# Optimization experiments

Hardware: AMD Instinct MI355X
Metric: run time of the kernel (lower is better)

## Reference

```python
import jax, jax.numpy as jnp
import numpy as np

N_PATHS, SEQ_LEN = 8192, 512
DATA_DIM, HIDDEN = 2, 128
MIN_VOL, MAX_VOL = 1e-4, 5.0


def setup_inputs() -> dict:
    key = jax.random.key(0)
    ks = jax.random.split(key, 10)
    def w(k, fin, fout, scale=1.0):
        return (jax.random.normal(k, (fin, fout), jnp.float32) * (scale / np.sqrt(fin))).astype(jnp.float32)
    # diffusion output bias init from the torch module: log(exp(target_vol) - 1 + 1e-8)
    gb3_init = float(np.log(np.exp(0.1) - 1.0 + 1e-8))
    return {
        "y0": jax.random.normal(ks[0], (N_PATHS, DATA_DIM), jnp.float32) * 0.1,
        "ts": jnp.arange(SEQ_LEN, dtype=jnp.float32),  # dt = 1.0 between outputs
        "dW": jax.random.normal(ks[1], (SEQ_LEN - 1, N_PATHS, DATA_DIM), jnp.float32),
        "fw1": w(ks[2], DATA_DIM + 1, HIDDEN), "fb1": jnp.zeros((HIDDEN,), jnp.float32),
        "fw2": w(ks[3], HIDDEN, HIDDEN),       "fb2": jnp.zeros((HIDDEN,), jnp.float32),
        "fw3": w(ks[4], HIDDEN, DATA_DIM, 0.02), "fb3": jnp.zeros((DATA_DIM,), jnp.float32),
        "gw1": w(ks[5], DATA_DIM, HIDDEN),     "gb1": jnp.zeros((HIDDEN,), jnp.float32),
        "gw2": w(ks[6], HIDDEN, HIDDEN),       "gb2": jnp.zeros((HIDDEN,), jnp.float32),
        "gw3": w(ks[7], HIDDEN, DATA_DIM, 0.02),
        "gb3": jnp.full((DATA_DIM,), gb3_init, jnp.float32),
    }


def _sde_paths(y0, ts, dW, fw1, fb1, fw2, fb2, fw3, fb3, gw1, gb1, gw2, gb2, gw3, gb3):
    def drift(y):  # f(t, y): MLP on [y, spread]
        spread = y[:, 0:1] - y[:, 1:2]
        h = jnp.concatenate([y, spread], axis=-1)            # [N, D+1]
        h = jax.nn.silu(h @ fw1 + fb1)
        h = jax.nn.silu(h @ fw2 + fb2)
        return h @ fw3 + fb3                                  # [N, D]

    def diffusion(y):  # g(t, y): softplus + clamp
        h = jax.nn.silu(y @ gw1 + gb1)
        h = jax.nn.silu(h @ gw2 + gb2)
        raw = h @ gw3 + gb3
        return jnp.clip(jax.nn.softplus(raw), MIN_VOL, MAX_VOL)  # [N, D]

    dts = ts[1:] - ts[:-1]  # [T-1]

    def step(y, inp):
        dw_std, dt = inp
        dw = dw_std * jnp.sqrt(dt)                 # Brownian increment ~ N(0, dt)
        f = drift(y)
        g, vjp_g = jax.vjp(diffusion, y)
        v = 0.5 * (dw * dw - dt)                   # Milstein weight (Ito)
        corr = vjp_g(v * g)[0]                     # torchsde autograd gdg_prod
        y1 = y + f * dt + g * dw + corr
        return y1, y1

    _, ys = jax.lax.scan(step, y0, (dW, dts))      # ys: [T-1, N, D]
    paths = jnp.concatenate([y0[None], ys], axis=0)  # [T, N, D]
    return jnp.transpose(paths, (1, 0, 2))           # [N, T, D]


def reference(y0, ts, dW, fw1, fb1, fw2, fb2, fw3, fb3, gw1, gb1, gw2, gb2, gw3, gb3):
    return _sde_paths(y0, ts, dW, fw1, fb1, fw2, fb2, fw3, fb3,
                      gw1, gb1, gw2, gb2, gw3, gb3)
```

## Files before the change

### kernel.cpp

```cpp
#include <hip/hip_runtime.h>
#include <math.h>

#define H      128
#define NPATH  8192
#define TLEN   512
#define BP     32
#define NTHR   512

typedef short bf16x8 __attribute__((ext_vector_type(8)));
typedef float f32x4  __attribute__((ext_vector_type(4)));

#define MFMA(a,b,c) __builtin_amdgcn_mfma_f32_16x16x32_bf16((a),(b),(c),0,0,0)

#define BAR() asm volatile("s_waitcnt lgkmcnt(0)\n\ts_barrier" ::: "memory")

#define O_WF2T  0
#define O_WG2T  32768
#define O_WG2R  65536
#define O_BFH   98304
#define O_BFL   106496
#define O_BGH   114688
#define O_BGL   122880
#define O_PF    131072
#define O_PRAW  132096
#define O_PCORR 133120
#define O_EP    134144
#define EP_FB2   0
#define EP_GB2   512
#define EP_W3F0  1024
#define EP_W3F1  1536
#define EP_W3G0  2048
#define EP_W3G1  2560
#define EP_GW1B0 3072
#define EP_GW1B1 3584
#define EP_GB1B  4096
#define O_TS    138752
#define SMEM_BYTES (O_TS + TLEN*4)

__device__ __forceinline__ float bf2f(unsigned v){ return __uint_as_float(v << 16); }
__device__ __forceinline__ unsigned short f2bf(float f){
  unsigned u = __float_as_uint(f);
  return (unsigned short)((u + 0x7fffu + ((u >> 16) & 1u)) >> 16);
}
__device__ __forceinline__ float ldany(const void* p, long long i, bool isbf){
  return isbf ? bf2f(((const unsigned short*)p)[i]) : ((const float*)p)[i];
}
__device__ __forceinline__ unsigned short ldbf(const void* p, long long i, bool isbf){
  return isbf ? ((const unsigned short*)p)[i] : f2bf(((const float*)p)[i]);
}
__device__ __forceinline__ float fsig(float x){
  return __builtin_amdgcn_rcpf(1.0f + __expf(-x));
}
__device__ __forceinline__ float fsilu(float x){ return x * fsig(x); }
__device__ __forceinline__ float fsilud(float x){
  float s = fsig(x); return s * (1.0f + x * (1.0f - s));
}
__device__ __forceinline__ float fsoftplus(float x){
  if (x > 15.0f) return x;
  return __logf(1.0f + __expf(x));
}
__device__ __forceinline__ unsigned cvtpk(float a, float b){
  unsigned r; asm("v_cvt_pk_bf16_f32 %0, %1, %2" : "=v"(r) : "v"(a), "v"(b)); return r;
}
__device__ __forceinline__ bf16x8 asfrag(uint4 u){
  union { uint4 u; bf16x8 b; } v; v.u = u; return v.b;
}

__global__ __launch_bounds__(NTHR, 2)
void GeneratorSDE_kernel(const void* __restrict__ y0, const void* __restrict__ ts,
                         const void* __restrict__ dW,
                         const void* __restrict__ fw1, const void* __restrict__ fb1,
                         const void* __restrict__ fw2, const void* __restrict__ fb2,
                         const void* __restrict__ fw3, const void* __restrict__ fb3,
                         const void* __restrict__ gw1, const void* __restrict__ gb1,
                         const void* __restrict__ gw2, const void* __restrict__ gb2,
                         const void* __restrict__ gw3, const void* __restrict__ gb3,
                         void* __restrict__ out)
{
  extern __shared__ char sm[];
  const int tid  = threadIdx.x;
  const int lane = tid & 63;
  const int w    = tid >> 6;
  const int wp   = w >> 1;
  const int nt   = w & 1;
  const int m16  = lane & 15;
  const int q    = lane >> 4;
  const int gpb  = blockIdx.x * BP;
  const int p1   = nt*16 + m16;
  const int gp   = gpb + p1;
  const int k8   = wp*32 + q*8;

  const bool isbf = (((const unsigned*)ts)[1] != 0x3f800000u);

  const int RACT  = O_BFH + ((q*32 + p1) << 4);
  const int WACT  = O_BFH + (((wp*4 + q)*32 + p1) << 4);
  const int WC2   = O_BFH + (((wp*4 + (q >> 1))*32 + p1) << 4) + ((q & 1) << 3);
  const int RAW   = O_WF2T + ((q*128 + wp*32 + m16) << 4);
  const int RAR   = O_WG2R + ((q*128 + wp*32 + m16) << 4);
  const int RPART = O_PF + (p1 << 3);
  const int WPART = O_PF + ((wp*32 + p1) << 3);
  const int REP   = O_EP + wp*128 + q*16;

  for (int e = tid; e < H * H; e += NTHR){
    int k = e >> 7, n = e & 127;
    unsigned short fv = ldbf(fw2, e, isbf);
    unsigned short gv = ldbf(gw2, e, isbf);
    *(unsigned short*)(sm + O_WF2T + (((k >> 3)*128 + n) << 4) + ((k & 7) << 1)) = fv;
    *(unsigned short*)(sm + O_WG2T + (((k >> 3)*128 + n) << 4) + ((k & 7) << 1)) = gv;
    *(unsigned short*)(sm + O_WG2R + (((n >> 3)*128 + k) << 4) + ((n & 7) << 1)) = gv;
  }
  if (tid < H){
    int e = tid;
    ((float*)(sm + O_EP + EP_FB2))[e]   = ldany(fb2, e, isbf);
    ((float*)(sm + O_EP + EP_GB2))[e]   = ldany(gb2, e, isbf);
    ((float*)(sm + O_EP + EP_W3F0))[e]  = ldany(fw3, 2*e + 0, isbf);
    ((float*)(sm + O_EP + EP_W3F1))[e]  = ldany(fw3, 2*e + 1, isbf);
    ((float*)(sm + O_EP + EP_W3G0))[e]  = ldany(gw3, 2*e + 0, isbf);
    ((float*)(sm + O_EP + EP_W3G1))[e]  = ldany(gw3, 2*e + 1, isbf);
    ((float*)(sm + O_EP + EP_GW1B0))[e] = ldany(gw1, e, isbf);
    ((float*)(sm + O_EP + EP_GW1B1))[e] = ldany(gw1, H + e, isbf);
    ((float*)(sm + O_EP + EP_GB1B))[e]  = ldany(gb1, e, isbf);
  }
  for (int e = tid; e < TLEN; e += NTHR)
    ((float*)(sm + O_TS))[e] = ldany(ts, e, isbf);

  float fw1a[8], fw1b[8], fb1r[8], gw1r0[8], gw1r1[8], gb1r[8];
  #pragma unroll
  for (int kk = 0; kk < 8; ++kk){
    int k = k8 + kk;
    float r0 = ldany(fw1, k, isbf), r1 = ldany(fw1, H + k, isbf), r2 = ldany(fw1, 2*H + k, isbf);
    fw1a[kk]  = r0 + r2;
    fw1b[kk]  = r1 - r2;
    fb1r[kk]  = ldany(fb1, k,     isbf);
    gw1r0[kk] = ldany(gw1, k,     isbf);
    gw1r1[kk] = ldany(gw1, H + k, isbf);
    gb1r[kk]  = ldany(gb1, k,     isbf);
  }
  const float fb3r0 = ldany(fb3, 0, isbf), fb3r1 = ldany(fb3, 1, isbf);
  const float gb3r0 = ldany(gb3, 0, isbf), gb3r1 = ldany(gb3, 1, isbf);

  float ycur0 = ldany(y0, (long long)gp*2 + 0, isbf);
  float ycur1 = ldany(y0, (long long)gp*2 + 1, isbf);
  if (w < 2 && lane < 16){
    size_t r = (size_t)gp * TLEN;
    if (isbf) ((unsigned*)out)[r] = (unsigned)f2bf(ycur0) | ((unsigned)f2bf(ycur1) << 16);
    else      ((float2*)out)[r]   = make_float2(ycur0, ycur1);
  }
  float2 dwcur;
  {
    long long e = (long long)gp * 2;
    if (isbf){ unsigned u = *(const unsigned*)((const unsigned short*)dW + e);
               dwcur = make_float2(bf2f(u & 0xffffu), bf2f(u >> 16)); }
    else       dwcur = *(const float2*)((const float*)dW + e);
  }
  __syncthreads();

  const float* TSf = (const float*)(sm + O_TS);

  for (int t = 0; t < TLEN - 1; ++t){
    float dt = TSf[t+1] - TSf[t];
    float sqdt = sqrtf(dt);

    float2 dwnext;
    {
      int tn = (t + 1 <= TLEN - 2) ? t + 1 : TLEN - 2;
      long long e = ((long long)tn * NPATH + gp) * 2;
      if (isbf){ unsigned u = *(const unsigned*)((const unsigned short*)dW + e);
                 dwnext = make_float2(bf2f(u & 0xffffu), bf2f(u >> 16)); }
      else       dwnext = *(const float2*)((const float*)dW + e);
    }

    {
      float hf[8], hg[8];
      #pragma unroll
      for (int kk = 0; kk < 8; ++kk){
        hf[kk] = fsilu(fb1r[kk] + ycur0*fw1a[kk]  + ycur1*fw1b[kk]);
        hg[kk] = fsilu(gb1r[kk] + ycur0*gw1r0[kk] + ycur1*gw1r1[kk]);
      }
      unsigned fh[4], fl[4], gh[4], gl[4];
      #pragma unroll
      for (int i = 0; i < 4; ++i){
        fh[i] = cvtpk(hf[2*i], hf[2*i+1]);
        gh[i] = cvtpk(hg[2*i], hg[2*i+1]);
        float f0 = __uint_as_float(fh[i] << 16), f1 = __uint_as_float(fh[i] & 0xffff0000u);
        float g0 = __uint_as_float(gh[i] << 16), g1 = __uint_as_float(gh[i] & 0xffff0000u);
        fl[i] = cvtpk(hf[2*i] - f0, hf[2*i+1] - f1);
        gl[i] = cvtpk(hg[2*i] - g0, hg[2*i+1] - g1);
      }
      *(uint4*)(sm + WACT        ) = make_uint4(fh[0], fh[1], fh[2], fh[3]);
      *(uint4*)(sm + WACT +  8192) = make_uint4(fl[0], fl[1], fl[2], fl[3]);
      *(uint4*)(sm + WACT + 16384) = make_uint4(gh[0], gh[1], gh[2], gh[3]);
      *(uint4*)(sm + WACT + 24576) = make_uint4(gl[0], gl[1], gl[2], gl[3]);
    }
    BAR();

    f32x4 accg[2];
    float sgr[8];
    f32x4 w3g0v[2], w3g1v[2];
    {
      f32x4 accf[2];
      accf[0] = (f32x4)0.f; accf[1] = (f32x4)0.f;
      accg[0] = (f32x4)0.f; accg[1] = (f32x4)0.f;
      #pragma unroll
      for (int kt = 0; kt < 4; ++kt){
        bf16x8 bfh = asfrag(*(const uint4*)(sm + RACT + kt*2048        ));
        bf16x8 bfl = asfrag(*(const uint4*)(sm + RACT + kt*2048 +  8192));
        bf16x8 bgh = asfrag(*(const uint4*)(sm + RACT + kt*2048 + 16384));
        bf16x8 bgl = asfrag(*(const uint4*)(sm + RACT + kt*2048 + 24576));
        bf16x8 af0 = asfrag(*(const uint4*)(sm + RAW + kt*8192        ));
        bf16x8 af1 = asfrag(*(const uint4*)(sm + RAW + kt*8192 +   256));
        bf16x8 ag0 = asfrag(*(const uint4*)(sm + RAW + kt*8192 + 32768));
        bf16x8 ag1 = asfrag(*(const uint4*)(sm + RAW + kt*8192 + 33024));
        accf[0] = MFMA(af0, bfl, accf[0]); accf[0] = MFMA(af0, bfh, accf[0]);
        accf[1] = MFMA(af1, bfl, accf[1]); accf[1] = MFMA(af1, bfh, accf[1]);
        accg[0] = MFMA(ag0, bgl, accg[0]); accg[0] = MFMA(ag0, bgh, accg[0]);
        accg[1] = MFMA(ag1, bgl, accg[1]); accg[1] = MFMA(ag1, bgh, accg[1]);
      }
      float pf0 = 0, pf1 = 0, pr0 = 0, pr1 = 0;
      #pragma unroll
      for (int mi = 0; mi < 2; ++mi){
        f32x4 fb2v  = *(const f32x4*)(sm + REP + mi*64 + EP_FB2);
        f32x4 gb2v  = *(const f32x4*)(sm + REP + mi*64 + EP_GB2);
        f32x4 w3f0v = *(const f32x4*)(sm + REP + mi*64 + EP_W3F0);
        f32x4 w3f1v = *(const f32x4*)(sm + REP + mi*64 + EP_W3F1);
        w3g0v[mi] = *(const f32x4*)(sm + REP + mi*64 + EP_W3G0);
        w3g1v[mi] = *(const f32x4*)(sm + REP + mi*64 + EP_W3G1);
        #pragma unroll
        for (int r = 0; r < 4; ++r){
          float vf = fsilu(accf[mi][r] + fb2v[r]);
          pf0 += vf * w3f0v[r];
          pf1 += vf * w3f1v[r];
          float zg = accg[mi][r] + gb2v[r];
          float s  = fsig(zg);
          accg[mi][r] = zg;
          sgr[mi*4+r] = s;
          float vg = zg * s;
          pr0 += vg * w3g0v[mi][r];
          pr1 += vg * w3g1v[mi][r];
        }
      }
      pf0 += __shfl_xor(pf0, 16, 64); pf0 += __shfl_xor(pf0, 32, 64);
      pf1 += __shfl_xor(pf1, 16, 64); pf1 += __shfl_xor(pf1, 32, 64);
      pr0 += __shfl_xor(pr0, 16, 64); pr0 += __shfl_xor(pr0, 32, 64);
      pr1 += __shfl_xor(pr1, 16, 64); pr1 += __shfl_xor(pr1, 32, 64);
      if (lane < 16){
        *(float2*)(sm + WPART       ) = make_float2(pf0, pf1);
        *(float2*)(sm + WPART + 1024) = make_float2(pr0, pr1);
      }
    }
    BAR();

    float g0, g1, dw0, dw1, cr0, cr1;
    {
      float raw0 = gb3r0, raw1 = gb3r1;
      #pragma unroll
      for (int w2 = 0; w2 < 4; ++w2){
        float2 v = *(const float2*)(sm + RPART + w2*256 + 1024);
        raw0 += v.x; raw1 += v.y;
      }
      dw0 = dwcur.x * sqdt; dw1 = dwcur.y * sqdt;
      float vv0 = 0.5f*(dw0*dw0 - dt), vv1 = 0.5f*(dw1*dw1 - dt);
      float sp0 = fsoftplus(raw0), sp1 = fsoftplus(raw1);
      g0 = fminf(fmaxf(sp0, 1e-4f), 5.0f);
      g1 = fminf(fmaxf(sp1, 1e-4f), 5.0f);
      float m0 = (sp0 > 1e-4f && sp0 < 5.0f) ? 1.0f : 0.0f;
      float m1 = (sp1 > 1e-4f && sp1 < 5.0f) ? 1.0f : 0.0f;
      cr0 = vv0 * (g0 * fsig(raw0) * m0);
      cr1 = vv1 * (g1 * fsig(raw1) * m1);
    }

    #pragma unroll
    for (int mi = 0; mi < 2; ++mi){
      float c2[4];
      #pragma unroll
      for (int r = 0; r < 4; ++r){
        float s = sgr[mi*4+r], z = accg[mi][r];
        float sd = s * (1.0f + z * (1.0f - s));
        c2[r] = (cr0 * w3g0v[mi][r] + cr1 * w3g1v[mi][r]) * sd;
      }
      unsigned h0 = cvtpk(c2[0], c2[1]), h1 = cvtpk(c2[2], c2[3]);
      float a0 = __uint_as_float(h0 << 16), a1 = __uint_as_float(h0 & 0xffff0000u);
      float a2 = __uint_as_float(h1 << 16), a3 = __uint_as_float(h1 & 0xffff0000u);
      unsigned l0 = cvtpk(c2[0] - a0, c2[1] - a1), l1 = cvtpk(c2[2] - a2, c2[3] - a3);
      *(uint2*)(sm + WC2 + mi*1024       ) = make_uint2(h0, h1);
      *(uint2*)(sm + WC2 + mi*1024 + 8192) = make_uint2(l0, l1);
    }
    BAR();

    {
      f32x4 accc[2];
      accc[0] = (f32x4)0.f; accc[1] = (f32x4)0.f;
      #pragma unroll
      for (int kt = 0; kt < 4; ++kt){
        bf16x8 bh = asfrag(*(const uint4*)(sm + RACT + kt*2048       ));
        bf16x8 bl = asfrag(*(const uint4*)(sm + RACT + kt*2048 + 8192));
        bf16x8 a0 = asfrag(*(const uint4*)(sm + RAR + kt*8192      ));
        bf16x8 a1 = asfrag(*(const uint4*)(sm + RAR + kt*8192 + 256));
        accc[0] = MFMA(a0, bl, accc[0]); accc[0] = MFMA(a0, bh, accc[0]);
        accc[1] = MFMA(a1, bl, accc[1]); accc[1] = MFMA(a1, bh, accc[1]);
      }
      float pc0 = 0, pc1 = 0;
      #pragma unroll
      for (int mi = 0; mi < 2; ++mi){
        f32x4 gb1v = *(const f32x4*)(sm + REP + mi*64 + EP_GB1B );
        f32x4 b0v  = *(const f32x4*)(sm + REP + mi*64 + EP_GW1B0);
        f32x4 b1v  = *(const f32x4*)(sm + REP + mi*64 + EP_GW1B1);
        #pragma unroll
        for (int r = 0; r < 4; ++r){
          float z1 = gb1v[r] + ycur0*b0v[r] + ycur1*b1v[r];
          float u  = accc[mi][r] * fsilud(z1);
          pc0 += u * b0v[r];
          pc1 += u * b1v[r];
        }
      }
      pc0 += __shfl_xor(pc0, 16, 64); pc0 += __shfl_xor(pc0, 32, 64);
      pc1 += __shfl_xor(pc1, 16, 64); pc1 += __shfl_xor(pc1, 32, 64);
      if (lane < 16)
        *(float2*)(sm + WPART + 2048) = make_float2(pc0, pc1);
    }
    BAR();

    {
      float f0 = fb3r0, f1 = fb3r1, c0 = 0.f, c1 = 0.f;
      #pragma unroll
      for (int w2 = 0; w2 < 4; ++w2){
        float2 a = *(const float2*)(sm + RPART + w2*256       );
        float2 b = *(const float2*)(sm + RPART + w2*256 + 2048);
        f0 += a.x; f1 += a.y; c0 += b.x; c1 += b.y;
      }
      ycur0 += f0*dt + g0*dw0 + c0;
      ycur1 += f1*dt + g1*dw1 + c1;
      if (w < 2 && lane < 16){
        size_t r = (size_t)gp * TLEN + (t + 1);
        if (isbf) ((unsigned*)out)[r] = (unsigned)f2bf(ycur0) | ((unsigned)f2bf(ycur1) << 16);
        else      ((float2*)out)[r]   = make_float2(ycur0, ycur1);
      }
      dwcur = dwnext;
    }
  }
}

extern "C" void kernel_launch(void* const* d_in, const int* in_sizes, int n_in,
                              void* d_out, int out_size, void* d_ws, size_t ws_size,
                              hipStream_t stream)
{
  (void)in_sizes; (void)n_in; (void)out_size; (void)d_ws; (void)ws_size;
  hipFuncSetAttribute((const void*)GeneratorSDE_kernel,
                      hipFuncAttributeMaxDynamicSharedMemorySize, SMEM_BYTES);
  GeneratorSDE_kernel<<<dim3(NPATH / BP), dim3(NTHR), SMEM_BYTES, stream>>>(
      d_in[0], d_in[1], d_in[2],
      d_in[3], d_in[4], d_in[5], d_in[6], d_in[7], d_in[8],
      d_in[9], d_in[10], d_in[11], d_in[12], d_in[13], d_in[14],
      d_out);
}
```

Baseline: 2.146 ms.

## Keep MLP weight fragments in registers instead of shared memory

Loads the fw2, gw2 and transposed gw2 MFMA A-fragments once into per-thread registers (96 VGPRs) instead of staging them in LDS and re-reading them every timestep. LDS use drops by about 96KB and launch bounds go from two blocks per CU to one, so more registers are available. The aim is to remove per-step LDS weight traffic from the serial scan. The cost is lower occupancy and possible register spills. Initial weight loads become strided global reads.

```diff
diff --git a/kernel.cpp b/kernel.cpp
--- a/kernel.cpp
+++ b/kernel.cpp
@@ -14,17 +14,14 @@
 
 #define BAR() asm volatile("s_waitcnt lgkmcnt(0)\n\ts_barrier" ::: "memory")
 
-#define O_WF2T  0
-#define O_WG2T  32768
-#define O_WG2R  65536
-#define O_BFH   98304
-#define O_BFL   106496
-#define O_BGH   114688
-#define O_BGL   122880
-#define O_PF    131072
-#define O_PRAW  132096
-#define O_PCORR 133120
-#define O_EP    134144
+#define O_BFH   0
+#define O_BFL   8192
+#define O_BGH   16384
+#define O_BGL   24576
+#define O_PF    32768
+#define O_PRAW  33792
+#define O_PCORR 34816
+#define O_EP    35840
 #define EP_FB2   0
 #define EP_GB2   512
 #define EP_W3F0  1024
@@ -34,7 +31,7 @@
 #define EP_GW1B0 3072
 #define EP_GW1B1 3584
 #define EP_GB1B  4096
-#define O_TS    138752
+#define O_TS    40448
 #define SMEM_BYTES (O_TS + TLEN*4)
 
 __device__ __forceinline__ float bf2f(unsigned v){ return __uint_as_float(v << 16); }
@@ -66,7 +63,7 @@
   union { uint4 u; bf16x8 b; } v; v.u = u; return v.b;
 }
 
-__global__ __launch_bounds__(NTHR, 2)
+__global__ __launch_bounds__(NTHR, 1)
 void GeneratorSDE_kernel(const void* __restrict__ y0, const void* __restrict__ ts,
                          const void* __restrict__ dW,
                          const void* __restrict__ fw1, const void* __restrict__ fb1,
@@ -95,20 +92,25 @@
   const int RACT  = O_BFH + ((q*32 + p1) << 4);
   const int WACT  = O_BFH + (((wp*4 + q)*32 + p1) << 4);
   const int WC2   = O_BFH + (((wp*4 + (q >> 1))*32 + p1) << 4) + ((q & 1) << 3);
-  const int RAW   = O_WF2T + ((q*128 + wp*32 + m16) << 4);
-  const int RAR   = O_WG2R + ((q*128 + wp*32 + m16) << 4);
   const int RPART = O_PF + (p1 << 3);
   const int WPART = O_PF + ((wp*32 + p1) << 3);
   const int REP   = O_EP + wp*128 + q*16;
 
-  for (int e = tid; e < H * H; e += NTHR){
-    int k = e >> 7, n = e & 127;
-    unsigned short fv = ldbf(fw2, e, isbf);
-    unsigned short gv = ldbf(gw2, e, isbf);
-    *(unsigned short*)(sm + O_WF2T + (((k >> 3)*128 + n) << 4) + ((k & 7) << 1)) = fv;
-    *(unsigned short*)(sm + O_WG2T + (((k >> 3)*128 + n) << 4) + ((k & 7) << 1)) = gv;
-    *(unsigned short*)(sm + O_WG2R + (((n >> 3)*128 + k) << 4) + ((n & 7) << 1)) = gv;
-  }
+  bf16x8 aF[2][4], aG[2][4], aR[2][4];
+  #pragma unroll
+  for (int mi = 0; mi < 2; ++mi)
+    #pragma unroll
+    for (int kt = 0; kt < 4; ++kt){
+      int row = 32*wp + 16*mi + m16;
+      #pragma unroll
+      for (int j = 0; j < 8; ++j){
+        int col = kt*32 + q*8 + j;
+        aF[mi][kt][j] = (short)ldbf(fw2, (long long)col*H + row, isbf);
+        aG[mi][kt][j] = (short)ldbf(gw2, (long long)col*H + row, isbf);
+        aR[mi][kt][j] = (short)ldbf(gw2, (long long)row*H + col, isbf);
+      }
+    }
+
   if (tid < H){
     int e = tid;
     ((float*)(sm + O_EP + EP_FB2))[e]   = ldany(fb2, e, isbf);
@@ -207,14 +209,10 @@
         bf16x8 bfl = asfrag(*(const uint4*)(sm + RACT + kt*2048 +  8192));
         bf16x8 bgh = asfrag(*(const uint4*)(sm + RACT + kt*2048 + 16384));
         bf16x8 bgl = asfrag(*(const uint4*)(sm + RACT + kt*2048 + 24576));
-        bf16x8 af0 = asfrag(*(const uint4*)(sm + RAW + kt*8192        ));
-        bf16x8 af1 = asfrag(*(const uint4*)(sm + RAW + kt*8192 +   256));
-        bf16x8 ag0 = asfrag(*(const uint4*)(sm + RAW + kt*8192 + 32768));
-        bf16x8 ag1 = asfrag(*(const uint4*)(sm + RAW + kt*8192 + 33024));
-        accf[0] = MFMA(af0, bfl, accf[0]); accf[0] = MFMA(af0, bfh, accf[0]);
-        accf[1] = MFMA(af1, bfl, accf[1]); accf[1] = MFMA(af1, bfh, accf[1]);
-        accg[0] = MFMA(ag0, bgl, accg[0]); accg[0] = MFMA(ag0, bgh, accg[0]);
-        accg[1] = MFMA(ag1, bgl, accg[1]); accg[1] = MFMA(ag1, bgh, accg[1]);
+        accf[0] = MFMA(aF[0][kt], bfl, accf[0]); accf[0] = MFMA(aF[0][kt], bfh, accf[0]);
+        accf[1] = MFMA(aF[1][kt], bfl, accf[1]); accf[1] = MFMA(aF[1][kt], bfh, accf[1]);
+        accg[0] = MFMA(aG[0][kt], bgl, accg[0]); accg[0] = MFMA(aG[0][kt], bgh, accg[0]);
+        accg[1] = MFMA(aG[1][kt], bgl, accg[1]); accg[1] = MFMA(aG[1][kt], bgh, accg[1]);
       }
       float pf0 = 0, pf1 = 0, pr0 = 0, pr1 = 0;
       #pragma unroll
@@ -294,10 +292,8 @@
       for (int kt = 0; kt < 4; ++kt){
         bf16x8 bh = asfrag(*(const uint4*)(sm + RACT + kt*2048       ));
         bf16x8 bl = asfrag(*(const uint4*)(sm + RACT + kt*2048 + 8192));
-        bf16x8 a0 = asfrag(*(const uint4*)(sm + RAR + kt*8192      ));
-        bf16x8 a1 = asfrag(*(const uint4*)(sm + RAR + kt*8192 + 256));
-        accc[0] = MFMA(a0, bl, accc[0]); accc[0] = MFMA(a0, bh, accc[0]);
-        accc[1] = MFMA(a1, bl, accc[1]); accc[1] = MFMA(a1, bh, accc[1]);
+        accc[0] = MFMA(aR[0][kt], bl, accc[0]); accc[0] = MFMA(aR[0][kt], bh, accc[0]);
+        accc[1] = MFMA(aR[1][kt], bl, accc[1]); accc[1] = MFMA(aR[1][kt], bh, accc[1]);
       }
       float pc0 = 0, pc1 = 0;
       #pragma unroll
```

Result: faster. 2.021 ms (-5.8%).

## Reschedule per-step stages to drop a barrier and overlap drift MFMA

Applied to the files above, without the earlier changes.

The drift layer-2 MFMA moves after the diffusion head, so it runs in the barrier window alongside the softplus and correction work. The backward VJP matmul is reorganised so each wave reads only the correction vector it wrote itself. That removes one block barrier per time step, and silu-derivatives are precomputed in the first stage and staged in a new shared-memory region. Layer-1 weights move from registers to shared memory, and launch bounds drop to one block per SM. This cuts occupancy and adds LDS traffic.

```diff
diff --git a/kernel.cpp b/kernel.cpp
--- a/kernel.cpp
+++ b/kernel.cpp
@@ -11,7 +11,6 @@
 typedef float f32x4  __attribute__((ext_vector_type(4)));
 
 #define MFMA(a,b,c) __builtin_amdgcn_mfma_f32_16x16x32_bf16((a),(b),(c),0,0,0)
-
 #define BAR() asm volatile("s_waitcnt lgkmcnt(0)\n\ts_barrier" ::: "memory")
 
 #define O_WF2T  0
@@ -34,7 +33,11 @@
 #define EP_GW1B0 3072
 #define EP_GW1B1 3584
 #define EP_GB1B  4096
-#define O_TS    138752
+#define EP_FW1A  4608
+#define EP_FW1B  5120
+#define EP_FB1   5632
+#define O_SD    140288
+#define O_TS    157184
 #define SMEM_BYTES (O_TS + TLEN*4)
 
 __device__ __forceinline__ float bf2f(unsigned v){ return __uint_as_float(v << 16); }
@@ -52,9 +55,6 @@
   return __builtin_amdgcn_rcpf(1.0f + __expf(-x));
 }
 __device__ __forceinline__ float fsilu(float x){ return x * fsig(x); }
-__device__ __forceinline__ float fsilud(float x){
-  float s = fsig(x); return s * (1.0f + x * (1.0f - s));
-}
 __device__ __forceinline__ float fsoftplus(float x){
   if (x > 15.0f) return x;
   return __logf(1.0f + __expf(x));
@@ -65,8 +65,9 @@
 __device__ __forceinline__ bf16x8 asfrag(uint4 u){
   union { uint4 u; bf16x8 b; } v; v.u = u; return v.b;
 }
-
-__global__ __launch_bounds__(NTHR, 2)
+#define LD4(off) (*(const f32x4*)(sm + (off)))
+
+__global__ __launch_bounds__(NTHR, 1)
 void GeneratorSDE_kernel(const void* __restrict__ y0, const void* __restrict__ ts,
                          const void* __restrict__ dW,
                          const void* __restrict__ fw1, const void* __restrict__ fb1,
@@ -92,14 +93,21 @@
 
   const bool isbf = (((const unsigned*)ts)[1] != 0x3f800000u);
 
-  const int RACT  = O_BFH + ((q*32 + p1) << 4);
+  const int RACTF = O_BFH + ((q*32 + p1) << 4);
+  const int RACTG = O_BGH + ((q*32 + p1) << 4);
+  const int RAF   = O_WF2T + ((q*128 + wp*32 + m16) << 4);
+  const int RAG   = O_WG2T + ((q*128 + wp*32 + m16) << 4);
+  const int RAB   = O_WG2R + (((4*wp + q)*128 + m16) << 4);
   const int WACT  = O_BFH + (((wp*4 + q)*32 + p1) << 4);
-  const int WC2   = O_BFH + (((wp*4 + (q >> 1))*32 + p1) << 4) + ((q & 1) << 3);
-  const int RAW   = O_WF2T + ((q*128 + wp*32 + m16) << 4);
-  const int RAR   = O_WG2R + ((q*128 + wp*32 + m16) << 4);
+  const int WC2   = O_BGH + (((wp*4 + (q>>1))*32 + p1) << 4) + ((q&1) << 3);
+  const int RC2   = O_BGH + (((4*wp + q)*32 + p1) << 4);
   const int RPART = O_PF + (p1 << 3);
   const int WPART = O_PF + ((wp*32 + p1) << 3);
   const int REP   = O_EP + wp*128 + q*16;
+  const int REPB  = O_EP + q*16;
+  const int RS0   = O_EP + (k8 << 2);
+  const int WSD   = O_SD + (p1*132 + k8)*4;
+  const int RSD   = O_SD + (p1*132 + 4*q)*4;
 
   for (int e = tid; e < H * H; e += NTHR){
     int k = e >> 7, n = e & 127;
@@ -111,6 +119,10 @@
   }
   if (tid < H){
     int e = tid;
+    float r0 = ldany(fw1, e, isbf), r1 = ldany(fw1, H + e, isbf), r2 = ldany(fw1, 2*H + e, isbf);
+    ((float*)(sm + O_EP + EP_FW1A))[e]  = r0 + r2;
+    ((float*)(sm + O_EP + EP_FW1B))[e]  = r1 - r2;
+    ((float*)(sm + O_EP + EP_FB1))[e]   = ldany(fb1, e, isbf);
     ((float*)(sm + O_EP + EP_FB2))[e]   = ldany(fb2, e, isbf);
     ((float*)(sm + O_EP + EP_GB2))[e]   = ldany(gb2, e, isbf);
     ((float*)(sm + O_EP + EP_W3F0))[e]  = ldany(fw3, 2*e + 0, isbf);
@@ -124,18 +136,6 @@
   for (int e = tid; e < TLEN; e += NTHR)
     ((float*)(sm + O_TS))[e] = ldany(ts, e, isbf);
 
-  float fw1a[8], fw1b[8], fb1r[8], gw1r0[8], gw1r1[8], gb1r[8];
-  #pragma unroll
-  for (int kk = 0; kk < 8; ++kk){
-    int k = k8 + kk;
-    float r0 = ldany(fw1, k, isbf), r1 = ldany(fw1, H + k, isbf), r2 = ldany(fw1, 2*H + k, isbf);
-    fw1a[kk]  = r0 + r2;
-    fw1b[kk]  = r1 - r2;
-    fb1r[kk]  = ldany(fb1, k,     isbf);
-    gw1r0[kk] = ldany(gw1, k,     isbf);
-    gw1r1[kk] = ldany(gw1, H + k, isbf);
-    gb1r[kk]  = ldany(gb1, k,     isbf);
-  }
   const float fb3r0 = ldany(fb3, 0, isbf), fb3r1 = ldany(fb3, 1, isbf);
   const float gb3r0 = ldany(gb3, 0, isbf), gb3r1 = ldany(gb3, 1, isbf);
 
@@ -171,11 +171,22 @@
     }
 
     {
-      float hf[8], hg[8];
+      f32x4 fav[2], fbv[2], f1v[2], ga[2], gb[2], g1[2];
+      fav[0] = LD4(RS0 + EP_FW1A);  fav[1] = LD4(RS0 + EP_FW1A + 16);
+      fbv[0] = LD4(RS0 + EP_FW1B);  fbv[1] = LD4(RS0 + EP_FW1B + 16);
+      f1v[0] = LD4(RS0 + EP_FB1);   f1v[1] = LD4(RS0 + EP_FB1  + 16);
+      ga[0]  = LD4(RS0 + EP_GW1B0); ga[1]  = LD4(RS0 + EP_GW1B0 + 16);
+      gb[0]  = LD4(RS0 + EP_GW1B1); gb[1]  = LD4(RS0 + EP_GW1B1 + 16);
+      g1[0]  = LD4(RS0 + EP_GB1B);  g1[1]  = LD4(RS0 + EP_GB1B  + 16);
+      float hf[8], hg[8], sd[8];
       #pragma unroll
       for (int kk = 0; kk < 8; ++kk){
-        hf[kk] = fsilu(fb1r[kk] + ycur0*fw1a[kk]  + ycur1*fw1b[kk]);
-        hg[kk] = fsilu(gb1r[kk] + ycur0*gw1r0[kk] + ycur1*gw1r1[kk]);
+        int v = kk >> 2, r = kk & 3;
+        float zf = f1v[v][r] + ycur0*fav[v][r] + ycur1*fbv[v][r];
+        float zg = g1[v][r]  + ycur0*ga[v][r]  + ycur1*gb[v][r];
+        float sf = fsig(zf); hf[kk] = zf * sf;
+        float sg = fsig(zg); hg[kk] = zg * sg;
+        sd[kk] = sg * (1.0f + zg * (1.0f - sg));
       }
       unsigned fh[4], fl[4], gh[4], gl[4];
       #pragma unroll
@@ -183,74 +194,57 @@
         fh[i] = cvtpk(hf[2*i], hf[2*i+1]);
         gh[i] = cvtpk(hg[2*i], hg[2*i+1]);
         float f0 = __uint_as_float(fh[i] << 16), f1 = __uint_as_float(fh[i] & 0xffff0000u);
-        float g0 = __uint_as_float(gh[i] << 16), g1 = __uint_as_float(gh[i] & 0xffff0000u);
+        float g0 = __uint_as_float(gh[i] << 16), g1_ = __uint_as_float(gh[i] & 0xffff0000u);
         fl[i] = cvtpk(hf[2*i] - f0, hf[2*i+1] - f1);
-        gl[i] = cvtpk(hg[2*i] - g0, hg[2*i+1] - g1);
+        gl[i] = cvtpk(hg[2*i] - g0, hg[2*i+1] - g1_);
       }
       *(uint4*)(sm + WACT        ) = make_uint4(fh[0], fh[1], fh[2], fh[3]);
       *(uint4*)(sm + WACT +  8192) = make_uint4(fl[0], fl[1], fl[2], fl[3]);
       *(uint4*)(sm + WACT + 16384) = make_uint4(gh[0], gh[1], gh[2], gh[3]);
       *(uint4*)(sm + WACT + 24576) = make_uint4(gl[0], gl[1], gl[2], gl[3]);
+      *(f32x4*)(sm + WSD         ) = (f32x4){sd[0], sd[1], sd[2], sd[3]};
+      *(f32x4*)(sm + WSD + 16    ) = (f32x4){sd[4], sd[5], sd[6], sd[7]};
     }
     BAR();
 
     f32x4 accg[2];
     float sgr[8];
-    f32x4 w3g0v[2], w3g1v[2];
-    {
-      f32x4 accf[2];
-      accf[0] = (f32x4)0.f; accf[1] = (f32x4)0.f;
+    {
       accg[0] = (f32x4)0.f; accg[1] = (f32x4)0.f;
       #pragma unroll
       for (int kt = 0; kt < 4; ++kt){
-        bf16x8 bfh = asfrag(*(const uint4*)(sm + RACT + kt*2048        ));
-        bf16x8 bfl = asfrag(*(const uint4*)(sm + RACT + kt*2048 +  8192));
-        bf16x8 bgh = asfrag(*(const uint4*)(sm + RACT + kt*2048 + 16384));
-        bf16x8 bgl = asfrag(*(const uint4*)(sm + RACT + kt*2048 + 24576));
-        bf16x8 af0 = asfrag(*(const uint4*)(sm + RAW + kt*8192        ));
-        bf16x8 af1 = asfrag(*(const uint4*)(sm + RAW + kt*8192 +   256));
-        bf16x8 ag0 = asfrag(*(const uint4*)(sm + RAW + kt*8192 + 32768));
-        bf16x8 ag1 = asfrag(*(const uint4*)(sm + RAW + kt*8192 + 33024));
-        accf[0] = MFMA(af0, bfl, accf[0]); accf[0] = MFMA(af0, bfh, accf[0]);
-        accf[1] = MFMA(af1, bfl, accf[1]); accf[1] = MFMA(af1, bfh, accf[1]);
+        bf16x8 bgh = asfrag(*(const uint4*)(sm + RACTG + kt*2048       ));
+        bf16x8 bgl = asfrag(*(const uint4*)(sm + RACTG + kt*2048 + 8192));
+        bf16x8 ag0 = asfrag(*(const uint4*)(sm + RAG + kt*8192      ));
+        bf16x8 ag1 = asfrag(*(const uint4*)(sm + RAG + kt*8192 + 256));
         accg[0] = MFMA(ag0, bgl, accg[0]); accg[0] = MFMA(ag0, bgh, accg[0]);
         accg[1] = MFMA(ag1, bgl, accg[1]); accg[1] = MFMA(ag1, bgh, accg[1]);
       }
-      float pf0 = 0, pf1 = 0, pr0 = 0, pr1 = 0;
+      float pr0 = 0, pr1 = 0;
       #pragma unroll
       for (int mi = 0; mi < 2; ++mi){
-        f32x4 fb2v  = *(const f32x4*)(sm + REP + mi*64 + EP_FB2);
-        f32x4 gb2v  = *(const f32x4*)(sm + REP + mi*64 + EP_GB2);
-        f32x4 w3f0v = *(const f32x4*)(sm + REP + mi*64 + EP_W3F0);
-        f32x4 w3f1v = *(const f32x4*)(sm + REP + mi*64 + EP_W3F1);
-        w3g0v[mi] = *(const f32x4*)(sm + REP + mi*64 + EP_W3G0);
-        w3g1v[mi] = *(const f32x4*)(sm + REP + mi*64 + EP_W3G1);
+        f32x4 gb2v  = LD4(REP + mi*64 + EP_GB2);
+        f32x4 w3g0v = LD4(REP + mi*64 + EP_W3G0);
+        f32x4 w3g1v = LD4(REP + mi*64 + EP_W3G1);
         #pragma unroll
         for (int r = 0; r < 4; ++r){
-          float vf = fsilu(accf[mi][r] + fb2v[r]);
-          pf0 += vf * w3f0v[r];
-          pf1 += vf * w3f1v[r];
           float zg = accg[mi][r] + gb2v[r];
           float s  = fsig(zg);
           accg[mi][r] = zg;
           sgr[mi*4+r] = s;
           float vg = zg * s;
-          pr0 += vg * w3g0v[mi][r];
-          pr1 += vg * w3g1v[mi][r];
+          pr0 += vg * w3g0v[r];
+          pr1 += vg * w3g1v[r];
         }
       }
-      pf0 += __shfl_xor(pf0, 16, 64); pf0 += __shfl_xor(pf0, 32, 64);
-      pf1 += __shfl_xor(pf1, 16, 64); pf1 += __shfl_xor(pf1, 32, 64);
       pr0 += __shfl_xor(pr0, 16, 64); pr0 += __shfl_xor(pr0, 32, 64);
       pr1 += __shfl_xor(pr1, 16, 64); pr1 += __shfl_xor(pr1, 32, 64);
-      if (lane < 16){
-        *(float2*)(sm + WPART       ) = make_float2(pf0, pf1);
+      if (lane < 16)
         *(float2*)(sm + WPART + 1024) = make_float2(pr0, pr1);
-      }
     }
     BAR();
 
-    float g0, g1, dw0, dw1, cr0, cr1;
+    float g0s, g1s, dw0, dw1;
     {
       float raw0 = gb3r0, raw1 = gb3r1;
       #pragma unroll
@@ -258,57 +252,79 @@
         float2 v = *(const float2*)(sm + RPART + w2*256 + 1024);
         raw0 += v.x; raw1 += v.y;
       }
+      f32x4 accf[2];
+      accf[0] = (f32x4)0.f; accf[1] = (f32x4)0.f;
+      #pragma unroll
+      for (int kt = 0; kt < 4; ++kt){
+        bf16x8 bfh = asfrag(*(const uint4*)(sm + RACTF + kt*2048       ));
+        bf16x8 bfl = asfrag(*(const uint4*)(sm + RACTF + kt*2048 + 8192));
+        bf16x8 af0 = asfrag(*(const uint4*)(sm + RAF + kt*8192      ));
+        bf16x8 af1 = asfrag(*(const uint4*)(sm + RAF + kt*8192 + 256));
+        accf[0] = MFMA(af0, bfl, accf[0]); accf[0] = MFMA(af0, bfh, accf[0]);
+        accf[1] = MFMA(af1, bfl, accf[1]); accf[1] = MFMA(af1, bfh, accf[1]);
+      }
       dw0 = dwcur.x * sqdt; dw1 = dwcur.y * sqdt;
       float vv0 = 0.5f*(dw0*dw0 - dt), vv1 = 0.5f*(dw1*dw1 - dt);
       float sp0 = fsoftplus(raw0), sp1 = fsoftplus(raw1);
-      g0 = fminf(fmaxf(sp0, 1e-4f), 5.0f);
-      g1 = fminf(fmaxf(sp1, 1e-4f), 5.0f);
+      g0s = fminf(fmaxf(sp0, 1e-4f), 5.0f);
+      g1s = fminf(fmaxf(sp1, 1e-4f), 5.0f);
       float m0 = (sp0 > 1e-4f && sp0 < 5.0f) ? 1.0f : 0.0f;
       float m1 = (sp1 > 1e-4f && sp1 < 5.0f) ? 1.0f : 0.0f;
-      cr0 = vv0 * (g0 * fsig(raw0) * m0);
-      cr1 = vv1 * (g1 * fsig(raw1) * m1);
-    }
-
-    #pragma unroll
-    for (int mi = 0; mi < 2; ++mi){
-      float c2[4];
-      #pragma unroll
-      for (int r = 0; r < 4; ++r){
-        float s = sgr[mi*4+r], z = accg[mi][r];
-        float sd = s * (1.0f + z * (1.0f - s));
-        c2[r] = (cr0 * w3g0v[mi][r] + cr1 * w3g1v[mi][r]) * sd;
-      }
-      unsigned h0 = cvtpk(c2[0], c2[1]), h1 = cvtpk(c2[2], c2[3]);
-      float a0 = __uint_as_float(h0 << 16), a1 = __uint_as_float(h0 & 0xffff0000u);
-      float a2 = __uint_as_float(h1 << 16), a3 = __uint_as_float(h1 & 0xffff0000u);
-      unsigned l0 = cvtpk(c2[0] - a0, c2[1] - a1), l1 = cvtpk(c2[2] - a2, c2[3] - a3);
-      *(uint2*)(sm + WC2 + mi*1024       ) = make_uint2(h0, h1);
-      *(uint2*)(sm + WC2 + mi*1024 + 8192) = make_uint2(l0, l1);
-    }
-    BAR();
-
-    {
-      f32x4 accc[2];
-      accc[0] = (f32x4)0.f; accc[1] = (f32x4)0.f;
-      #pragma unroll
-      for (int kt = 0; kt < 4; ++kt){
-        bf16x8 bh = asfrag(*(const uint4*)(sm + RACT + kt*2048       ));
-        bf16x8 bl = asfrag(*(const uint4*)(sm + RACT + kt*2048 + 8192));
-        bf16x8 a0 = asfrag(*(const uint4*)(sm + RAR + kt*8192      ));
-        bf16x8 a1 = asfrag(*(const uint4*)(sm + RAR + kt*8192 + 256));
-        accc[0] = MFMA(a0, bl, accc[0]); accc[0] = MFMA(a0, bh, accc[0]);
-        accc[1] = MFMA(a1, bl, accc[1]); accc[1] = MFMA(a1, bh, accc[1]);
-      }
-      float pc0 = 0, pc1 = 0;
+      float cr0 = vv0 * (g0s * fsig(raw0) * m0);
+      float cr1 = vv1 * (g1s * fsig(raw1) * m1);
       #pragma unroll
       for (int mi = 0; mi < 2; ++mi){
-        f32x4 gb1v = *(const f32x4*)(sm + REP + mi*64 + EP_GB1B );
-        f32x4 b0v  = *(const f32x4*)(sm + REP + mi*64 + EP_GW1B0);
-        f32x4 b1v  = *(const f32x4*)(sm + REP + mi*64 + EP_GW1B1);
+        f32x4 w3g0v = LD4(REP + mi*64 + EP_W3G0);
+        f32x4 w3g1v = LD4(REP + mi*64 + EP_W3G1);
+        float c2[4];
         #pragma unroll
         for (int r = 0; r < 4; ++r){
-          float z1 = gb1v[r] + ycur0*b0v[r] + ycur1*b1v[r];
-          float u  = accc[mi][r] * fsilud(z1);
+          float s = sgr[mi*4+r], z = accg[mi][r];
+          float sd2 = s * (1.0f + z * (1.0f - s));
+          c2[r] = (cr0 * w3g0v[r] + cr1 * w3g1v[r]) * sd2;
+        }
+        unsigned h0 = cvtpk(c2[0], c2[1]), h1 = cvtpk(c2[2], c2[3]);
+        float a0 = __uint_as_float(h0 << 16), a1 = __uint_as_float(h0 & 0xffff0000u);
+        float a2 = __uint_as_float(h1 << 16), a3 = __uint_as_float(h1 & 0xffff0000u);
+        unsigned l0 = cvtpk(c2[0] - a0, c2[1] - a1), l1 = cvtpk(c2[2] - a2, c2[3] - a3);
+        *(uint2*)(sm + WC2 + mi*1024       ) = make_uint2(h0, h1);
+        *(uint2*)(sm + WC2 + mi*1024 + 8192) = make_uint2(l0, l1);
+      }
+      {
+        float pf0 = 0, pf1 = 0;
+        #pragma unroll
+        for (int mi = 0; mi < 2; ++mi){
+          f32x4 fb2v  = LD4(REP + mi*64 + EP_FB2);
+          f32x4 w3f0v = LD4(REP + mi*64 + EP_W3F0);
+          f32x4 w3f1v = LD4(REP + mi*64 + EP_W3F1);
+          #pragma unroll
+          for (int r = 0; r < 4; ++r){
+            float vf = fsilu(accf[mi][r] + fb2v[r]);
+            pf0 += vf * w3f0v[r];
+            pf1 += vf * w3f1v[r];
+          }
+        }
+        pf0 += __shfl_xor(pf0, 16, 64); pf0 += __shfl_xor(pf0, 32, 64);
+        pf1 += __shfl_xor(pf1, 16, 64); pf1 += __shfl_xor(pf1, 32, 64);
+        if (lane < 16)
+          *(float2*)(sm + WPART) = make_float2(pf0, pf1);
+      }
+      asm volatile("s_waitcnt lgkmcnt(0)" ::: "memory");
+      bf16x8 ch = asfrag(*(const uint4*)(sm + RC2       ));
+      bf16x8 cl = asfrag(*(const uint4*)(sm + RC2 + 8192));
+      float pc0 = 0, pc1 = 0;
+      #pragma unroll
+      for (int mi = 0; mi < 8; ++mi){
+        bf16x8 a = asfrag(*(const uint4*)(sm + RAB + mi*256));
+        f32x4 accc = (f32x4)0.f;
+        accc = MFMA(a, cl, accc);
+        accc = MFMA(a, ch, accc);
+        f32x4 sdv = LD4(RSD  + mi*64);
+        f32x4 b0v = LD4(REPB + mi*64 + EP_GW1B0);
+        f32x4 b1v = LD4(REPB + mi*64 + EP_GW1B1);
+        #pragma unroll
+        for (int r = 0; r < 4; ++r){
+          float u = accc[r] * sdv[r];
           pc0 += u * b0v[r];
           pc1 += u * b1v[r];
         }
@@ -328,8 +344,8 @@
         float2 b = *(const float2*)(sm + RPART + w2*256 + 2048);
         f0 += a.x; f1 += a.y; c0 += b.x; c1 += b.y;
       }
-      ycur0 += f0*dt + g0*dw0 + c0;
-      ycur1 += f1*dt + g1*dw1 + c1;
+      ycur0 += f0*dt + g0s*dw0 + c0;
+      ycur1 += f1*dt + g1s*dw1 + c1;
       if (w < 2 && lane < 16){
         size_t r = (size_t)gp * TLEN + (t + 1);
         if (isbf) ((unsigned*)out)[r] = (unsigned)f2bf(ycur0) | ((unsigned)f2bf(ycur1) << 16);
```

Result: slower. 2.330 ms (+8.6%).
